# Optimization experiments

Hardware: AMD Instinct MI355X
Metric: run time of the kernel (lower is better)

Reference implementation:

```python
import jax, jax.numpy as jnp
import numpy as np

# Grouped TF->gene sparse decoder dims
T = 512       # number of TFs (tf_size)
K = 4         # nodes_per_tf (width_multiplier); decoder_features = T*K = 2048
G = 20000     # number of genes (gene_size)
EPG = 3       # regulating TFs per gene (TF-gene edges per gene)
B = 512       # batch of cells


def setup_inputs() -> dict:
    key = jax.random.key(0)
    k0, k1, k2, k3, k4, k5, k6 = jax.random.split(key, 7)
    features = jax.random.normal(k0, (B, T), dtype=jnp.float32)
    # Layer 1: each TF fans out to its own K hidden nodes (one weight per edge)
    w1 = jax.random.normal(k1, (T, K), dtype=jnp.float32) * 0.5
    b1 = jax.random.normal(k2, (T, K), dtype=jnp.float32) * 0.1
    # Layer 2: block-dense KxK mixing within each TF group
    w2 = jax.random.normal(k3, (T, K, K), dtype=jnp.float32) * (1.0 / np.sqrt(K))
    b2 = jax.random.normal(k4, (T, K), dtype=jnp.float32) * 0.1
    # Output layer: gene g sums over its EPG TF edges x K hidden nodes
    w3 = jax.random.normal(k5, (G, EPG, K), dtype=jnp.float32) * (1.0 / np.sqrt(EPG * K))
    b3 = jax.random.normal(k6, (G,), dtype=jnp.float32) * 0.1
    # Fixed irregular TF-gene connectivity (constant structure, like data_obj)
    edge_tf = jnp.asarray(
        np.random.default_rng(0).integers(0, T, size=(G, EPG)), dtype=jnp.int32
    )
    return {"features": features, "w1": w1, "b1": b1, "w2": w2, "b2": b2,
            "w3": w3, "b3": b3, "edge_tf": edge_tf}


def reference(features, w1, b1, w2, b2, w3, b3, edge_tf):
    # SparseLinear decoder_1: TF t -> its K hidden nodes, then LeakyReLU(0.01)
    h1 = jax.nn.leaky_relu(features[:, :, None] * w1 + b1)            # [B,T,K]
    # SparseLinear decoder_2: block-dense within each TF group + LeakyReLU
    h2 = jax.nn.leaky_relu(jnp.einsum('btj,tjk->btk', h1, w2) + b2)   # [B,T,K]
    # SparseLinear output: gather each gene's regulating TF groups, contract
    gathered = h2[:, edge_tf, :]                                      # [B,G,EPG,K]
    out = jnp.einsum('bgek,gek->bg', gathered, w3) + b3               # [B,G]
    return out
```

## Files before the change

### kernel.cpp

```cpp
#include <hip/hip_runtime.h>

namespace {

constexpr int T = 512;
constexpr int K = 4;
constexpr int G = 20000;
constexpr int EPG = 3;
constexpr int B = 512;
constexpr int GC = 16;
constexpr int NGB = G / GC;
constexpr int LPAD = 20;
constexpr float SLOPE = 0.01f;
constexpr size_t H2T_OFF = 2u << 20;

__device__ __forceinline__ float lrelu(float x) { return x > 0.0f ? x : SLOPE * x; }

__global__ __launch_bounds__(256) void h2t_kernel(
    const float* __restrict__ features, const float* __restrict__ w1,
    const float* __restrict__ b1, const float* __restrict__ w2,
    const float* __restrict__ b2, float* __restrict__ h2t) {
  const int t = blockIdx.x;
  const int b = blockIdx.y * 256 + threadIdx.x;
  const float f = features[(size_t)b * T + t];
  const float4 W1 = reinterpret_cast<const float4*>(w1)[t];
  const float4 B1 = reinterpret_cast<const float4*>(b1)[t];
  const float4 B2 = reinterpret_cast<const float4*>(b2)[t];
  const float h0 = lrelu(f * W1.x + B1.x);
  const float h1 = lrelu(f * W1.y + B1.y);
  const float h2 = lrelu(f * W1.z + B1.z);
  const float h3 = lrelu(f * W1.w + B1.w);
  const float4* W2 = reinterpret_cast<const float4*>(w2 + (size_t)t * (K * K));
  const float4 r0 = W2[0];
  const float4 r1 = W2[1];
  const float4 r2 = W2[2];
  const float4 r3 = W2[3];
  float4 o;
  o.x = lrelu(B2.x + h0 * r0.x + h1 * r1.x + h2 * r2.x + h3 * r3.x);
  o.y = lrelu(B2.y + h0 * r0.y + h1 * r1.y + h2 * r2.y + h3 * r3.y);
  o.z = lrelu(B2.z + h0 * r0.z + h1 * r1.z + h2 * r2.z + h3 * r3.z);
  o.w = lrelu(B2.w + h0 * r0.w + h1 * r1.w + h2 * r2.w + h3 * r3.w);
  reinterpret_cast<float4*>(h2t)[(size_t)t * B + b] = o;
}

__global__ __launch_bounds__(256) void prep_kernel(
    const float* __restrict__ w3, const float* __restrict__ b3,
    const int* __restrict__ edge, float4* __restrict__ rec) {
  const int g = blockIdx.x * 256 + threadIdx.x;
  if (g >= G) return;
  const float4* wp = reinterpret_cast<const float4*>(w3 + (size_t)g * (EPG * K));
  const float4 a = wp[0], b = wp[1], c = wp[2];
  float4 d;
  d.x = b3[g];
  d.y = __int_as_float(edge[g * EPG + 0] * (B * K * 4));
  d.z = __int_as_float(edge[g * EPG + 1] * (B * K * 4));
  d.w = __int_as_float(edge[g * EPG + 2] * (B * K * 4));
  float4* o = rec + (size_t)g * 4;
  o[0] = a; o[1] = b; o[2] = c; o[3] = d;
}

__global__ __launch_bounds__(256) void out_kernel_v3(
    const float* __restrict__ h2t, const float4* __restrict__ rec,
    float* __restrict__ out) {
  __shared__ float lds[256 * LPAD];
  const int tid = threadIdx.x;
  const int g0 = blockIdx.x * GC;
  const char* h2b = reinterpret_cast<const char*>(h2t) +
                    ((size_t)blockIdx.y * 256 + tid) * 16;
  float acc[GC];
#pragma unroll
  for (int gi = 0; gi < GC; ++gi) {
    const float4* r = rec + (size_t)(g0 + gi) * 4;
    const float4 w0 = r[0];
    const float4 w1v = r[1];
    const float4 w2v = r[2];
    const float4 m = r[3];
    const float4 v0 = *reinterpret_cast<const float4*>(h2b + __float_as_int(m.y));
    const float4 v1 = *reinterpret_cast<const float4*>(h2b + __float_as_int(m.z));
    const float4 v2 = *reinterpret_cast<const float4*>(h2b + __float_as_int(m.w));
    float a = m.x;
    a += v0.x * w0.x + v0.y * w0.y + v0.z * w0.z + v0.w * w0.w;
    a += v1.x * w1v.x + v1.y * w1v.y + v1.z * w1v.z + v1.w * w1v.w;
    a += v2.x * w2v.x + v2.y * w2v.y + v2.z * w2v.z + v2.w * w2v.w;
    acc[gi] = a;
  }
#pragma unroll
  for (int q = 0; q < GC / 4; ++q)
    *reinterpret_cast<float4*>(&lds[tid * LPAD + q * 4]) =
        make_float4(acc[q * 4 + 0], acc[q * 4 + 1], acc[q * 4 + 2], acc[q * 4 + 3]);
  __syncthreads();
#pragma unroll
  for (int j = 0; j < GC; ++j) {
    const int flat = j * 256 + tid;
    const int brow = flat >> 4;
    const int gcol = flat & 15;
    out[((size_t)blockIdx.y * 256 + brow) * G + g0 + gcol] = lds[brow * LPAD + gcol];
  }
}

}

extern "C" void kernel_launch(void* const* d_in, const int* in_sizes, int n_in,
                              void* d_out, int out_size, void* d_ws, size_t ws_size,
                              hipStream_t stream) {
  const float* features = (const float*)d_in[0];
  const float* w1 = (const float*)d_in[1];
  const float* b1 = (const float*)d_in[2];
  const float* w2 = (const float*)d_in[3];
  const float* b2 = (const float*)d_in[4];
  const float* w3 = (const float*)d_in[5];
  const float* b3 = (const float*)d_in[6];
  const int* edge = (const int*)d_in[7];
  float* out = (float*)d_out;

  float4* rec = (float4*)d_ws;
  float* h2t = (float*)((char*)d_ws + H2T_OFF);

  dim3 g1(T, B / 256);
  h2t_kernel<<<g1, 256, 0, stream>>>(features, w1, b1, w2, b2, h2t);

  prep_kernel<<<(G + 255) / 256, 256, 0, stream>>>(w3, b3, edge, rec);

  dim3 g2(NGB, B / 256);
  out_kernel_v3<<<g2, 256, 0, stream>>>(h2t, rec, out);
}
```

Before: 107.6 us.

## Stage per-batch-tile h2 slices in LDS and keep gene weights in registers

The output kernel now loads a 4-batch slice of the full h2 table into shared memory with direct global-to-LDS loads. The 3 TF gathers per gene then run against LDS instead of global memory. Each thread holds the weights for 4 genes in registers across 8 batch tiles, and prep pads the gene records to a multiple of 256. This removes the scattered global gathers but reloads 32 KB per tile per block, with no overlap between loading and compute, and the random LDS reads can hit bank conflicts.

```diff
diff --git a/kernel.cpp b/kernel.cpp
--- a/kernel.cpp
+++ b/kernel.cpp
@@ -7,9 +7,12 @@
 constexpr int G = 20000;
 constexpr int EPG = 3;
 constexpr int B = 512;
-constexpr int GC = 16;
-constexpr int NGB = G / GC;
-constexpr int LPAD = 20;
+constexpr int GB = 256;
+constexpr int NXB = (G + GB - 1) / GB;
+constexpr int GPAD = NXB * GB;
+constexpr int BT = 4;
+constexpr int NYB = 16;
+constexpr int NTILE = B / (BT * NYB);
 constexpr float SLOPE = 0.01f;
 constexpr size_t H2T_OFF = 2u << 20;
 
@@ -46,54 +49,79 @@
     const float* __restrict__ w3, const float* __restrict__ b3,
     const int* __restrict__ edge, float4* __restrict__ rec) {
   const int g = blockIdx.x * 256 + threadIdx.x;
-  if (g >= G) return;
-  const float4* wp = reinterpret_cast<const float4*>(w3 + (size_t)g * (EPG * K));
-  const float4 a = wp[0], b = wp[1], c = wp[2];
-  float4 d;
-  d.x = b3[g];
-  d.y = __int_as_float(edge[g * EPG + 0] * (B * K * 4));
-  d.z = __int_as_float(edge[g * EPG + 1] * (B * K * 4));
-  d.w = __int_as_float(edge[g * EPG + 2] * (B * K * 4));
+  float4 a = make_float4(0.f, 0.f, 0.f, 0.f), b = a, c = a, d = a;
+  if (g < G) {
+    const float4* wp = reinterpret_cast<const float4*>(w3 + (size_t)g * (EPG * K));
+    a = wp[0];
+    b = wp[1];
+    c = wp[2];
+    d.x = b3[g];
+    d.y = __int_as_float(edge[g * EPG + 0] * (BT * K * 4));
+    d.z = __int_as_float(edge[g * EPG + 1] * (BT * K * 4));
+    d.w = __int_as_float(edge[g * EPG + 2] * (BT * K * 4));
+  } else {
+    d.y = d.z = d.w = __int_as_float(0);
+  }
   float4* o = rec + (size_t)g * 4;
   o[0] = a; o[1] = b; o[2] = c; o[3] = d;
 }
 
-__global__ __launch_bounds__(256) void out_kernel_v3(
+__global__ __launch_bounds__(256, 4) void out_kernel_v4(
     const float* __restrict__ h2t, const float4* __restrict__ rec,
     float* __restrict__ out) {
-  __shared__ float lds[256 * LPAD];
+  __shared__ float lds[BT * T * K];
   const int tid = threadIdx.x;
-  const int g0 = blockIdx.x * GC;
-  const char* h2b = reinterpret_cast<const char*>(h2t) +
-                    ((size_t)blockIdx.y * 256 + tid) * 16;
-  float acc[GC];
+  const int gsub = tid >> 2;
+  const int bidx = tid & 3;
+  const int wid = tid >> 6;
+  const int g0 = blockIdx.x * GB;
+  const int b0 = blockIdx.y * (BT * NTILE);
+
+  float4 rw0[4], rw1[4], rw2[4], rm[4];
 #pragma unroll
-  for (int gi = 0; gi < GC; ++gi) {
-    const float4* r = rec + (size_t)(g0 + gi) * 4;
-    const float4 w0 = r[0];
-    const float4 w1v = r[1];
-    const float4 w2v = r[2];
-    const float4 m = r[3];
-    const float4 v0 = *reinterpret_cast<const float4*>(h2b + __float_as_int(m.y));
-    const float4 v1 = *reinterpret_cast<const float4*>(h2b + __float_as_int(m.z));
-    const float4 v2 = *reinterpret_cast<const float4*>(h2b + __float_as_int(m.w));
-    float a = m.x;
-    a += v0.x * w0.x + v0.y * w0.y + v0.z * w0.z + v0.w * w0.w;
-    a += v1.x * w1v.x + v1.y * w1v.y + v1.z * w1v.z + v1.w * w1v.w;
-    a += v2.x * w2v.x + v2.y * w2v.y + v2.z * w2v.z + v2.w * w2v.w;
-    acc[gi] = a;
+  for (int s = 0; s < 4; ++s) {
+    const float4* r = rec + (size_t)(g0 + s * 64 + gsub) * 4;
+    rw0[s] = r[0]; rw1[s] = r[1]; rw2[s] = r[2]; rm[s] = r[3];
   }
+  int off0[4], off1[4], off2[4];
 #pragma unroll
-  for (int q = 0; q < GC / 4; ++q)
-    *reinterpret_cast<float4*>(&lds[tid * LPAD + q * 4]) =
-        make_float4(acc[q * 4 + 0], acc[q * 4 + 1], acc[q * 4 + 2], acc[q * 4 + 3]);
-  __syncthreads();
+  for (int s = 0; s < 4; ++s) {
+    off0[s] = __float_as_int(rm[s].y) + bidx * 16;
+    off1[s] = __float_as_int(rm[s].z) + bidx * 16;
+    off2[s] = __float_as_int(rm[s].w) + bidx * 16;
+  }
+
+  const char* ldsc = reinterpret_cast<const char*>(lds);
+
+  for (int ib = 0; ib < NTILE; ++ib) {
+    const int bb = b0 + ib * BT;
 #pragma unroll
-  for (int j = 0; j < GC; ++j) {
-    const int flat = j * 256 + tid;
-    const int brow = flat >> 4;
-    const int gcol = flat & 15;
-    out[((size_t)blockIdx.y * 256 + brow) * G + g0 + gcol] = lds[brow * LPAD + gcol];
+    for (int j = 0; j < 8; ++j) {
+      const int idx = j * 256 + tid;
+      const int t = idx >> 2;
+      const int b = idx & 3;
+      const float* src = h2t + ((size_t)t * B + bb + b) * 4;
+      char* dst = reinterpret_cast<char*>(lds) + (j * 256 + wid * 64) * 16;
+      __builtin_amdgcn_global_load_lds(
+          (const __attribute__((address_space(1))) void*)src,
+          (__attribute__((address_space(3))) void*)dst, 16, 0, 0);
+    }
+    asm volatile("s_waitcnt vmcnt(0)" ::: "memory");
+    __syncthreads();
+
+#pragma unroll
+    for (int s = 0; s < 4; ++s) {
+      const float4 v0 = *reinterpret_cast<const float4*>(ldsc + off0[s]);
+      const float4 v1 = *reinterpret_cast<const float4*>(ldsc + off1[s]);
+      const float4 v2 = *reinterpret_cast<const float4*>(ldsc + off2[s]);
+      float a = rm[s].x;
+      a += v0.x * rw0[s].x + v0.y * rw0[s].y + v0.z * rw0[s].z + v0.w * rw0[s].w;
+      a += v1.x * rw1[s].x + v1.y * rw1[s].y + v1.z * rw1[s].z + v1.w * rw1[s].w;
+      a += v2.x * rw2[s].x + v2.y * rw2[s].y + v2.z * rw2[s].z + v2.w * rw2[s].w;
+      const int g = g0 + s * 64 + gsub;
+      if (g < G) out[(size_t)(bb + bidx) * G + g] = a;
+    }
+    __syncthreads();
   }
 }
 
@@ -118,8 +146,8 @@
   dim3 g1(T, B / 256);
   h2t_kernel<<<g1, 256, 0, stream>>>(features, w1, b1, w2, b2, h2t);
 
-  prep_kernel<<<(G + 255) / 256, 256, 0, stream>>>(w3, b3, edge, rec);
+  prep_kernel<<<GPAD / 256, 256, 0, stream>>>(w3, b3, edge, rec);
 
-  dim3 g2(NGB, B / 256);
-  out_kernel_v3<<<g2, 256, 0, stream>>>(h2t, rec, out);
+  dim3 g2(NXB, NYB);
+  out_kernel_v4<<<g2, 256, 0, stream>>>(h2t, rec, out);
 }
```

Result: slower. 114.9 us (+6.8%).
